# Optimization experiments

Measured on AMD Instinct MI355X. Metric: run time of the kernel, lower is better.

The kernel has to match this reference:

```python
import jax, jax.numpy as jnp
import numpy as np

N, MAX_NB, H, L, V, B, M = 16384, 15, 512, 128, 1024, 256, 65536


def setup_inputs() -> dict:
    key = jax.random.key(0)
    ks = jax.random.split(key, 32)
    s = 0.02  # param init scale
    inp = {
        'x_ids': jax.random.randint(ks[0], (N,), 0, V, dtype=jnp.int32),
        'contexts': jax.random.randint(ks[1], (N,), 0, B, dtype=jnp.int32),
        'nei_idx': jax.random.randint(ks[2], (N, MAX_NB), 0, M, dtype=jnp.int32),
        'nei_mask': jax.random.randint(ks[3], (N, MAX_NB), 0, 2, dtype=jnp.int32),
        'o_idx': jax.random.randint(ks[4], (N, MAX_NB), 0, M, dtype=jnp.int32),
        'o_mask': jax.random.randint(ks[5], (N, MAX_NB), 0, 2, dtype=jnp.int32),
        'H_msg': jax.random.normal(ks[6], (M, H), jnp.float32),
        'x_tree_vecs': jax.random.normal(ks[7], (B, L), jnp.float32),
        'embedding': jax.random.normal(ks[8], (V, H), jnp.float32) * s,
        'Wz_w': jax.random.normal(ks[9], (H, 2 * H), jnp.float32) * s,
        'Wz_b': jnp.zeros((H,), jnp.float32),
        'Wr_w': jax.random.normal(ks[10], (H, H), jnp.float32) * s,
        'Wr_b': jnp.zeros((H,), jnp.float32),
        'Ur_w': jax.random.normal(ks[11], (H, H), jnp.float32) * s,
        'Wh_w': jax.random.normal(ks[12], (H, 2 * H), jnp.float32) * s,
        'Wh_b': jnp.zeros((H,), jnp.float32),
        'W_w': jax.random.normal(ks[13], (H, H + L), jnp.float32) * s,
        'W_b': jnp.zeros((H,), jnp.float32),
        'Wo_w': jax.random.normal(ks[14], (V, H), jnp.float32) * s,
        'Wo_b': jnp.zeros((V,), jnp.float32),
        'Ui_w': jax.random.normal(ks[15], (H, 2 * H), jnp.float32) * s,
        'Ui_b': jnp.zeros((H,), jnp.float32),
        'U_w': jax.random.normal(ks[16], (H, H + L), jnp.float32) * s,
        'U_b': jnp.zeros((H,), jnp.float32),
        'Uo_w': jax.random.normal(ks[17], (1, H), jnp.float32) * s,
        'Uo_b': jnp.zeros((1,), jnp.float32),
    }
    return inp


def _gru(x, h_nei, Wz_w, Wz_b, Wr_w, Wr_b, Ur_w, Wh_w, Wh_b):
    # x: [N,H], h_nei: [N,MAX_NB,H]
    sum_h = h_nei.sum(axis=1)
    z = jax.nn.sigmoid(jnp.concatenate([x, sum_h], axis=1) @ Wz_w.T + Wz_b)
    r1 = (x @ Wr_w.T + Wr_b)[:, None, :]          # [N,1,H]
    r2 = jnp.einsum('nkh,gh->nkg', h_nei, Ur_w)   # U_r(h_nei), no bias
    r = jax.nn.sigmoid(r1 + r2)
    sum_gated = (r * h_nei).sum(axis=1)
    pre_h = jnp.tanh(jnp.concatenate([x, sum_gated], axis=1) @ Wh_w.T + Wh_b)
    return (1.0 - z) * sum_h + z * pre_h


def reference(x_ids, contexts, nei_idx, nei_mask, o_idx, o_mask, H_msg,
              x_tree_vecs, embedding, Wz_w, Wz_b, Wr_w, Wr_b, Ur_w,
              Wh_w, Wh_b, W_w, W_b, Wo_w, Wo_b, Ui_w, Ui_b, U_w, U_b,
              Uo_w, Uo_b):
    x = embedding[x_ids]                                   # [N,H]
    h_nei = H_msg[nei_idx] * nei_mask[..., None].astype(H_msg.dtype)  # [N,NB,H]
    o_nei = H_msg[o_idx] * o_mask[..., None].astype(H_msg.dtype)
    new_h = _gru(x, h_nei, Wz_w, Wz_b, Wr_w, Wr_b, Ur_w, Wh_w, Wh_b)
    cur_o = o_nei.sum(axis=1)                              # [N,H]
    ctx = x_tree_vecs[contexts]                            # [N,L]
    # word prediction: aggregate(new_h, contexts, x_tree_vecs, 'word')
    w_hid = jax.nn.relu(jnp.concatenate([new_h, ctx], axis=1) @ W_w.T + W_b)
    word_scores = w_hid @ Wo_w.T + Wo_b                    # [N,V]
    # stop prediction: U_i(cat(x, cur_o)) -> aggregate(..., 'stop')
    stop_h = jax.nn.relu(jnp.concatenate([x, cur_o], axis=1) @ Ui_w.T + Ui_b)
    s_hid = jax.nn.relu(jnp.concatenate([stop_h, ctx], axis=1) @ U_w.T + U_b)
    stop_scores = s_hid @ Uo_w.T + Uo_b                    # [N,1]
    return jnp.concatenate([word_scores, stop_scores], axis=1)  # [N,V+1]
```

## Files before the change

kernel.cpp:

```cpp
#include <hip/hip_runtime.h>
#include <hip/hip_bf16.h>

typedef unsigned short u16;
typedef unsigned int u32;
typedef __attribute__((ext_vector_type(8))) short s8v;
typedef __attribute__((ext_vector_type(4))) float f4v;

#define HDIM 512
#define NNODE 16384
#define NB 15

__device__ __forceinline__ u16 f2bu(float x) {
  union { float f; u32 i; } v; v.f = x;
  u32 r = v.i + 0x7FFFu + ((v.i >> 16) & 1u);
  return (u16)(r >> 16);
}
__device__ __forceinline__ float bu2f(u16 u) {
  union { u32 i; float f; } v; v.i = ((u32)u) << 16;
  return v.f;
}
__device__ __forceinline__ u32 pk(float a, float b) {
  return (u32)f2bu(a) | ((u32)f2bu(b) << 16);
}
__device__ __forceinline__ float sigm(float x) {
  return __builtin_amdgcn_rcpf(1.f + __expf(-x));
}
__device__ __forceinline__ void gl16(const void* g, void* l) {
  __builtin_amdgcn_global_load_lds(
      (const __attribute__((address_space(1))) u32*)g,
      (__attribute__((address_space(3))) u32*)l, 16, 0, 0);
}
template<int N> __device__ __forceinline__ void wait_vm() {
  if constexpr (N == 0) asm volatile("s_waitcnt vmcnt(0)" ::: "memory");
  else if constexpr (N == 2) asm volatile("s_waitcnt vmcnt(2)" ::: "memory");
  else asm volatile("s_waitcnt vmcnt(4)" ::: "memory");
}

__global__ __launch_bounds__(256) void k_cvt_all(
    const float* Wz_w, const float* Wr_w, const float* Wh_w, const float* Ui_w,
    const float* Ur_w, const float* W_w, const float* U_w, const float* Wo_w,
    const float* emb, const float* xtree,
    const float* Wz_b, const float* Wr_b, const float* Wh_b, const float* Ui_b,
    const float* W_b, const float* U_b,
    u16* wcat, u16* wz_h, u16* wh_h, u16* ui_h, u16* ur, u16* w_n, u16* u_n,
    u16* ccat, u16* wo, u16* emb_bf, u16* xt_bf, float* ebias, float* cbias) {
  int seg = blockIdx.y;
  const float* src = nullptr; u16* dst = nullptr;
  const float* fsrc = nullptr; float* fdst = nullptr;
  int R = 0, Cs = 0, c0 = 0, C = 0, fn = 0;
  switch (seg) {
    case 0:  src = Wz_w; dst = wcat;              R = 512;  Cs = 1024; c0 = 0;   C = 512; break;
    case 1:  src = Wr_w; dst = wcat + 512 * 512;  R = 512;  Cs = 512;  c0 = 0;   C = 512; break;
    case 2:  src = Wh_w; dst = wcat + 1024 * 512; R = 512;  Cs = 1024; c0 = 0;   C = 512; break;
    case 3:  src = Ui_w; dst = wcat + 1536 * 512; R = 512;  Cs = 1024; c0 = 0;   C = 512; break;
    case 4:  src = Wz_w; dst = wz_h;              R = 512;  Cs = 1024; c0 = 512; C = 512; break;
    case 5:  src = Wh_w; dst = wh_h;              R = 512;  Cs = 1024; c0 = 512; C = 512; break;
    case 6:  src = Ui_w; dst = ui_h;              R = 512;  Cs = 1024; c0 = 512; C = 512; break;
    case 7:  src = Ur_w; dst = ur;                R = 512;  Cs = 512;  c0 = 0;   C = 512; break;
    case 8:  src = W_w;  dst = w_n;               R = 512;  Cs = 640;  c0 = 0;   C = 512; break;
    case 9:  src = U_w;  dst = u_n;               R = 512;  Cs = 640;  c0 = 0;   C = 512; break;
    case 10: src = W_w;  dst = ccat;              R = 512;  Cs = 640;  c0 = 512; C = 128; break;
    case 11: src = U_w;  dst = ccat + 512 * 128;  R = 512;  Cs = 640;  c0 = 512; C = 128; break;
    case 12: src = Wo_w; dst = wo;                R = 1024; Cs = 512;  c0 = 0;   C = 512; break;
    case 13: src = emb;  dst = emb_bf;            R = 1024; Cs = 512;  c0 = 0;   C = 512; break;
    case 14: src = xtree; dst = xt_bf;            R = 256;  Cs = 128;  c0 = 0;   C = 128; break;
    case 15: fsrc = Wz_b; fdst = ebias;        fn = 512; break;
    case 16: fsrc = Wr_b; fdst = ebias + 512;  fn = 512; break;
    case 17: fsrc = Wh_b; fdst = ebias + 1024; fn = 512; break;
    case 18: fsrc = Ui_b; fdst = ebias + 1536; fn = 512; break;
    case 19: fsrc = W_b;  fdst = cbias;        fn = 512; break;
    case 20: fsrc = U_b;  fdst = cbias + 512;  fn = 512; break;
  }
  int i = blockIdx.x * 256 + threadIdx.x;
  if (fdst) { if (i < fn) fdst[i] = fsrc[i]; return; }
  int e0 = i * 8;
  if (e0 >= R * C) return;
  int r = e0 / C, c = e0 - r * C;
  const float* s = src + (size_t)r * Cs + c0 + c;
  float4 a = *reinterpret_cast<const float4*>(s);
  float4 b = *reinterpret_cast<const float4*>(s + 4);
  uint4 o = {pk(a.x, a.y), pk(a.z, a.w), pk(b.x, b.y), pk(b.z, b.w)};
  *reinterpret_cast<uint4*>(&dst[e0]) = o;
}

__global__ void k_cvtH(const float* __restrict__ src, u16* __restrict__ HR) {
  size_t i = ((size_t)blockIdx.x * 256 + threadIdx.x) * 8;
  size_t m = i >> 9, c = i & 511;
  float4 a = *reinterpret_cast<const float4*>(src + i);
  float4 b = *reinterpret_cast<const float4*>(src + i + 4);
  uint4 o = {pk(a.x, a.y), pk(a.z, a.w), pk(b.x, b.y), pk(b.z, b.w)};
  *reinterpret_cast<uint4*>(&HR[m * 1024 + c]) = o;
}

struct GP {
  const u16* A; const u16* B; int K; int lda;
  const float* gadd; int ldg; const int* gidx;
  const float* bias; const u16* shb;
  float* outf; u16* outh; int ldo;
};

template<int EP>
__device__ __forceinline__ void epi(int row, int col, float v, const GP& g) {
  if constexpr (EP == 0) {
    g.outf[(size_t)row * g.ldo + col] = v + (g.bias ? g.bias[col] : 0.f);
  } else if constexpr (EP == 3) {
    float pre = v + g.gadd[(size_t)g.gidx[row] * g.ldg + col];
    g.outh[(size_t)row * g.ldo + col] = f2bu(pre > 0.f ? pre : 0.f);
  } else {
    g.outh[(size_t)row * g.ldo + col] = f2bu(v);
  }
}

template<int EP, int KV>
__device__ void gemm_core(const GP& g, u16* AsB, u16* BsB) {
  const int tid = threadIdx.x, lane = tid & 63, w = tid >> 6;
  const int wm = (w >> 2) * 64, wn = (w & 3) * 32;
  const int nx = gridDim.x;
  int orig = blockIdx.y * nx + blockIdx.x;
  int q = (nx * gridDim.y) >> 3;
  int tile = (orig & 7) * q + (orig >> 3);
  const int n0 = (tile % nx) * 128, m0 = (tile / nx) * 128;

  const int sr = tid >> 2, sc = (tid & 3) ^ ((sr >> 1) & 3);
  const u16* gA = g.A + (size_t)(m0 + sr) * g.lda + sc * 8;
  const u16* gB = g.B + (size_t)(n0 + sr) * KV + sc * 8;
  const int ls = tid * 8;

  f4v acc[4][2];
  f4v z4 = {0.f, 0.f, 0.f, 0.f};
#pragma unroll
  for (int a = 0; a < 4; a++) { acc[a][0] = z4; acc[a][1] = z4; }

  constexpr int T = KV / 32;
  auto STAGE = [&](int t) {
    int buf = (t & 3) * 4096;
    gl16(gA + t * 32, AsB + buf + ls);
    gl16(gB + t * 32, BsB + buf + ls);
  };
  STAGE(0); STAGE(1); STAGE(2);

#pragma unroll
  for (int t = 0; t < T; t++) {
    if (t < T - 2) wait_vm<4>();
    else if (t == T - 2) wait_vm<2>();
    else wait_vm<0>();
    __builtin_amdgcn_s_barrier();
    asm volatile("" ::: "memory");
    if (t + 3 < T) STAGE(t + 3);
    const u16* as = AsB + (t & 3) * 4096;
    const u16* bs = BsB + (t & 3) * 4096;
    s8v af[4], bf[2];
    int cc = lane >> 4;
#pragma unroll
    for (int i = 0; i < 4; i++) {
      int R = wm + i * 16 + (lane & 15);
      af[i] = *reinterpret_cast<const s8v*>(
          &as[R * 32 + (cc ^ ((R >> 1) & 3)) * 8]);
    }
#pragma unroll
    for (int i = 0; i < 2; i++) {
      int C = wn + i * 16 + (lane & 15);
      bf[i] = *reinterpret_cast<const s8v*>(
          &bs[C * 32 + (cc ^ ((C >> 1) & 3)) * 8]);
    }
    __builtin_amdgcn_s_setprio(1);
#pragma unroll
    for (int mi = 0; mi < 4; mi++)
#pragma unroll
      for (int ni = 0; ni < 2; ni++)
        acc[mi][ni] = __builtin_amdgcn_mfma_f32_16x16x32_bf16(
            af[mi], bf[ni], acc[mi][ni], 0, 0, 0);
    __builtin_amdgcn_s_setprio(0);
  }
#pragma unroll
  for (int mi = 0; mi < 4; mi++)
#pragma unroll
    for (int ni = 0; ni < 2; ni++)
#pragma unroll
      for (int r = 0; r < 4; r++) {
        int row = m0 + wm + mi * 16 + (lane >> 4) * 4 + r;
        int col = n0 + wn + ni * 16 + (lane & 15);
        epi<EP>(row, col, acc[mi][ni][r], g);
      }
}

template<int EP, int KV>
__global__ __launch_bounds__(512, 4) void k_gemm(GP g) {
  __shared__ u16 As[4 * 4096], Bs[4 * 4096];
  gemm_core<EP, KV>(g, As, Bs);
}

template<int EPa, int EPb, int KV>
__global__ __launch_bounds__(512, 4) void k_pair(GP a, GP b) {
  __shared__ u16 As[4 * 4096], Bs[4 * 4096];
  if (blockIdx.z == 0) gemm_core<EPa, KV>(a, As, Bs);
  else gemm_core<EPb, KV>(b, As, Bs);
}

__global__ __launch_bounds__(512, 4) void k_znp(
    const u16* __restrict__ sumh, const u16* __restrict__ sg,
    const u16* __restrict__ Wz, const u16* __restrict__ Wh,
    const float* __restrict__ E_z, const float* __restrict__ E_h, int ldg,
    const int* __restrict__ gidx, u16* __restrict__ newh, GP gs) {
  __shared__ u16 S[32768];
  if (blockIdx.z == 1) { gemm_core<3, 512>(gs, S, S + 16384); return; }
  const int tid = threadIdx.x, lane = tid & 63, w = tid >> 6;
  const int wm = (w >> 2) * 64, wn = (w & 3) * 32;
  const int nx = gridDim.x;
  int orig = blockIdx.y * nx + blockIdx.x;
  int q = (nx * gridDim.y) >> 3;
  int tile = (orig & 7) * q + (orig >> 3);
  const int n0 = (tile % nx) * 128, m0 = (tile / nx) * 128;

  const int sr = tid >> 2, sc = (tid & 3) ^ ((sr >> 1) & 3);
  const u16* gA1 = sumh + (size_t)(m0 + sr) * HDIM + sc * 8;
  const u16* gA2 = sg + (size_t)(m0 + sr) * HDIM + sc * 8;
  const u16* gB1 = Wz + (size_t)(n0 + sr) * HDIM + sc * 8;
  const u16* gB2 = Wh + (size_t)(n0 + sr) * HDIM + sc * 8;
  const int ls = tid * 8;
  auto STAGE = [&](int t) {
    u16* base = S + (t & 1) * 16384;
    int k0 = t * 32;
    gl16(gA1 + k0, base + ls);
    gl16(gB1 + k0, base + 4096 + ls);
    gl16(gA2 + k0, base + 8192 + ls);
    gl16(gB2 + k0, base + 12288 + ls);
  };

  f4v az[4][2], ah[4][2];
  f4v z4 = {0.f, 0.f, 0.f, 0.f};
#pragma unroll
  for (int a = 0; a < 4; a++) {
    az[a][0] = z4; az[a][1] = z4; ah[a][0] = z4; ah[a][1] = z4;
  }

  STAGE(0);
#pragma unroll
  for (int t = 0; t < 16; t++) {
    __syncthreads();
    if (t + 1 < 16) STAGE(t + 1);
    const u16* base = S + (t & 1) * 16384;
    const u16* As1 = base, *Bs1 = base + 4096;
    const u16* As2 = base + 8192, *Bs2 = base + 12288;
    int cc = lane >> 4;
    {
      s8v af[4], bf[2];
#pragma unroll
      for (int i = 0; i < 4; i++) {
        int R = wm + i * 16 + (lane & 15);
        af[i] = *reinterpret_cast<const s8v*>(
            &As1[R * 32 + (cc ^ ((R >> 1) & 3)) * 8]);
      }
#pragma unroll
      for (int i = 0; i < 2; i++) {
        int C = wn + i * 16 + (lane & 15);
        bf[i] = *reinterpret_cast<const s8v*>(
            &Bs1[C * 32 + (cc ^ ((C >> 1) & 3)) * 8]);
      }
      __builtin_amdgcn_s_setprio(1);
#pragma unroll
      for (int mi = 0; mi < 4; mi++)
#pragma unroll
        for (int ni = 0; ni < 2; ni++)
          az[mi][ni] = __builtin_amdgcn_mfma_f32_16x16x32_bf16(
              af[mi], bf[ni], az[mi][ni], 0, 0, 0);
      __builtin_amdgcn_s_setprio(0);
    }
    {
      s8v af[4], bf[2];
#pragma unroll
      for (int i = 0; i < 4; i++) {
        int R = wm + i * 16 + (lane & 15);
        af[i] = *reinterpret_cast<const s8v*>(
            &As2[R * 32 + (cc ^ ((R >> 1) & 3)) * 8]);
      }
#pragma unroll
      for (int i = 0; i < 2; i++) {
        int C = wn + i * 16 + (lane & 15);
        bf[i] = *reinterpret_cast<const s8v*>(
            &Bs2[C * 32 + (cc ^ ((C >> 1) & 3)) * 8]);
      }
      __builtin_amdgcn_s_setprio(1);
#pragma unroll
      for (int mi = 0; mi < 4; mi++)
#pragma unroll
        for (int ni = 0; ni < 2; ni++)
          ah[mi][ni] = __builtin_amdgcn_mfma_f32_16x16x32_bf16(
              af[mi], bf[ni], ah[mi][ni], 0, 0, 0);
      __builtin_amdgcn_s_setprio(0);
    }
  }
#pragma unroll
  for (int mi = 0; mi < 4; mi++)
#pragma unroll
    for (int r = 0; r < 4; r++) {
      int row = m0 + wm + mi * 16 + (lane >> 4) * 4 + r;
      int xid = gidx[row];
      const float* ez = E_z + (size_t)xid * ldg;
      const float* eh = E_h + (size_t)xid * ldg;
#pragma unroll
      for (int ni = 0; ni < 2; ni++) {
        int col = n0 + wn + ni * 16 + (lane & 15);
        float zv = sigm(az[mi][ni][r] + ez[col]);
        float pre = tanhf(ah[mi][ni][r] + eh[col]);
        float sh = bu2f(sumh[(size_t)row * HDIM + col]);
        newh[(size_t)row * HDIM + col] = f2bu((1.f - zv) * sh + zv * pre);
      }
    }
}

__global__ __launch_bounds__(256) void k_gsr(
    const u16* __restrict__ HR,
    const float* __restrict__ E_r, int ldg, const int* __restrict__ x_ids,
    const int* __restrict__ nei_idx, const int* __restrict__ nei_mask,
    const int* __restrict__ o_idx, const int* __restrict__ o_mask,
    u16* __restrict__ sum_h_bf, u16* __restrict__ sg_bf,
    u16* __restrict__ cur_o_bf) {
  int t = threadIdx.x;
  int nd = t >> 6, lane = t & 63;
  int n = blockIdx.x * 4 + nd;
  __shared__ int sidx[4][NB], smsk[4][NB], soid[4][NB], somk[4][NB];
  __shared__ int sx[4];
  if (t < 60) {
    int nn = t / 15, k = t - nn * 15;
    size_t gofs = (size_t)(blockIdx.x * 4 + nn) * NB + k;
    sidx[nn][k] = nei_idx[gofs];
    smsk[nn][k] = nei_mask[gofs];
  } else if (t >= 64 && t < 124) {
    int tt = t - 64;
    int nn = tt / 15, k = tt - nn * 15;
    size_t gofs = (size_t)(blockIdx.x * 4 + nn) * NB + k;
    soid[nn][k] = o_idx[gofs];
    somk[nn][k] = o_mask[gofs];
  } else if (t >= 128 && t < 132) {
    sx[t - 128] = x_ids[blockIdx.x * 4 + (t - 128)];
  }
  __syncthreads();
  int c = lane * 8;
  const float* er = E_r + (size_t)sx[nd] * ldg + c;
  float4 e0 = *reinterpret_cast<const float4*>(er);
  float4 e1 = *reinterpret_cast<const float4*>(er + 4);
  float ev[8] = {e0.x, e0.y, e0.z, e0.w, e1.x, e1.y, e1.z, e1.w};
  float s[8], gg[8], oo[8];
#pragma unroll
  for (int i = 0; i < 8; i++) { s[i] = 0.f; gg[i] = 0.f; oo[i] = 0.f; }
#pragma unroll
  for (int k = 0; k < NB; k++) {
    if (smsk[nd][k]) {
      const u16* row = HR + (size_t)sidx[nd][k] * 1024 + c;
      uint4 hv = *reinterpret_cast<const uint4*>(row);
      uint4 rv = *reinterpret_cast<const uint4*>(row + 512);
      u32 ha[4] = {hv.x, hv.y, hv.z, hv.w};
      u32 ra[4] = {rv.x, rv.y, rv.z, rv.w};
#pragma unroll
      for (int p = 0; p < 4; p++) {
        float h0 = bu2f((u16)ha[p]), h1 = bu2f((u16)(ha[p] >> 16));
        s[p * 2] += h0; s[p * 2 + 1] += h1;
        gg[p * 2] += sigm(bu2f((u16)ra[p]) + ev[p * 2]) * h0;
        gg[p * 2 + 1] += sigm(bu2f((u16)(ra[p] >> 16)) + ev[p * 2 + 1]) * h1;
      }
    }
    if (somk[nd][k]) {
      uint4 ov = *reinterpret_cast<const uint4*>(
          HR + (size_t)soid[nd][k] * 1024 + c);
      u32 oa[4] = {ov.x, ov.y, ov.z, ov.w};
#pragma unroll
      for (int p = 0; p < 4; p++) {
        oo[p * 2] += bu2f((u16)oa[p]);
        oo[p * 2 + 1] += bu2f((u16)(oa[p] >> 16));
      }
    }
  }
  size_t b = (size_t)n * HDIM + c;
  uint4 ps = {pk(s[0], s[1]), pk(s[2], s[3]), pk(s[4], s[5]), pk(s[6], s[7])};
  uint4 pg = {pk(gg[0], gg[1]), pk(gg[2], gg[3]), pk(gg[4], gg[5]), pk(gg[6], gg[7])};
  uint4 po = {pk(oo[0], oo[1]), pk(oo[2], oo[3]), pk(oo[4], oo[5]), pk(oo[6], oo[7])};
  *reinterpret_cast<uint4*>(&sum_h_bf[b]) = ps;
  *reinterpret_cast<uint4*>(&sg_bf[b]) = pg;
  *reinterpret_cast<uint4*>(&cur_o_bf[b]) = po;
}

__global__ __launch_bounds__(512, 4) void k_wordstop(
    GP wgp, const u16* __restrict__ shid, const float* __restrict__ Uo_w,
    const float* __restrict__ Uo_b, float* __restrict__ out) {
  __shared__ u16 As[4 * 4096], Bs[4 * 4096];
  if (blockIdx.z == 0) { gemm_core<0, 512>(wgp, As, Bs); return; }
  int b = blockIdx.y * gridDim.x + blockIdx.x;
  int wv = threadIdx.x >> 6, lane = threadIdx.x & 63;
#pragma unroll
  for (int i = 0; i < 2; i++) {
    int n = b * 16 + wv * 2 + i;
    const u16* row = shid + (size_t)n * HDIM + lane * 8;
    const float* uw = Uo_w + lane * 8;
    uint4 v = *reinterpret_cast<const uint4*>(row);
    float4 u0 = *reinterpret_cast<const float4*>(uw);
    float4 u1 = *reinterpret_cast<const float4*>(uw + 4);
    float s = bu2f((u16)v.x) * u0.x + bu2f((u16)(v.x >> 16)) * u0.y +
              bu2f((u16)v.y) * u0.z + bu2f((u16)(v.y >> 16)) * u0.w +
              bu2f((u16)v.z) * u1.x + bu2f((u16)(v.z >> 16)) * u1.y +
              bu2f((u16)v.w) * u1.z + bu2f((u16)(v.w >> 16)) * u1.w;
#pragma unroll
    for (int off = 32; off; off >>= 1) s += __shfl_xor(s, off, 64);
    if (lane == 0) out[(size_t)n * 1025 + 1024] = s + Uo_b[0];
  }
}

extern "C" void kernel_launch(void* const* d_in, const int* in_sizes, int n_in,
                              void* d_out, int out_size, void* d_ws, size_t ws_size,
                              hipStream_t stream) {
  const int* x_ids = (const int*)d_in[0];
  const int* contexts = (const int*)d_in[1];
  const int* nei_idx = (const int*)d_in[2];
  const int* nei_mask = (const int*)d_in[3];
  const int* o_idx = (const int*)d_in[4];
  const int* o_mask = (const int*)d_in[5];
  const float* H_msg = (const float*)d_in[6];
  const float* xtree = (const float*)d_in[7];
  const float* emb = (const float*)d_in[8];
  const float* Wz_w = (const float*)d_in[9];  const float* Wz_b = (const float*)d_in[10];
  const float* Wr_w = (const float*)d_in[11]; const float* Wr_b = (const float*)d_in[12];
  const float* Ur_w = (const float*)d_in[13];
  const float* Wh_w = (const float*)d_in[14]; const float* Wh_b = (const float*)d_in[15];
  const float* W_w  = (const float*)d_in[16]; const float* W_b  = (const float*)d_in[17];
  const float* Wo_w = (const float*)d_in[18]; const float* Wo_b = (const float*)d_in[19];
  const float* Ui_w = (const float*)d_in[20]; const float* Ui_b = (const float*)d_in[21];
  const float* U_w  = (const float*)d_in[22]; const float* U_b  = (const float*)d_in[23];
  const float* Uo_w = (const float*)d_in[24]; const float* Uo_b = (const float*)d_in[25];
  float* out = (float*)d_out;
  const int M = 65536;

  char* base = (char*)d_ws;
  size_t ofs = 0;
  auto alloc = [&](size_t bytes) -> char* {
    char* p = base + ofs;
    ofs = (ofs + bytes + 255) & ~(size_t)255;
    return p;
  };
  u16* wcat  = (u16*)alloc((size_t)2048 * 512 * 2);
  u16* wz_h  = (u16*)alloc(512 * 512 * 2);
  u16* wh_h  = (u16*)alloc(512 * 512 * 2);
  u16* ui_h  = (u16*)alloc(512 * 512 * 2);
  u16* ur    = (u16*)alloc(512 * 512 * 2);
  u16* w_n   = (u16*)alloc(512 * 512 * 2);
  u16* u_n   = (u16*)alloc(512 * 512 * 2);
  u16* ccat  = (u16*)alloc(1024 * 128 * 2);
  u16* wo    = (u16*)alloc(1024 * 512 * 2);
  u16* emb_bf = (u16*)alloc(1024 * 512 * 2);
  u16* xt_bf  = (u16*)alloc(256 * 128 * 2);
  float* ebias = (float*)alloc(2048 * 4);
  float* cbias = (float*)alloc(1024 * 4);
  float* E_cat = (float*)alloc((size_t)1024 * 2048 * 4);
  float* C_cat = (float*)alloc((size_t)256 * 1024 * 4);
  u16* HR = (u16*)alloc((size_t)M * 1024 * 2);
  u16* sum_h_bf = (u16*)alloc((size_t)NNODE * HDIM * 2);
  u16* cur_o_bf = (u16*)alloc((size_t)NNODE * HDIM * 2);
  u16* sg_bf    = (u16*)alloc((size_t)NNODE * HDIM * 2);
  u16* newh_bf  = (u16*)alloc((size_t)NNODE * HDIM * 2);
  u16* whid_bf  = (u16*)alloc((size_t)NNODE * HDIM * 2);
  u16* stoph_bf = (u16*)alloc((size_t)NNODE * HDIM * 2);
  u16* shid_bf  = (u16*)alloc((size_t)NNODE * HDIM * 2);

  k_cvt_all<<<dim3(256, 21), dim3(256), 0, stream>>>(
      Wz_w, Wr_w, Wh_w, Ui_w, Ur_w, W_w, U_w, Wo_w, emb, xtree,
      Wz_b, Wr_b, Wh_b, Ui_b, W_b, U_b,
      wcat, wz_h, wh_h, ui_h, ur, w_n, u_n, ccat, wo, emb_bf, xt_bf,
      ebias, cbias);
  k_cvtH<<<dim3(16384), dim3(256), 0, stream>>>(H_msg, HR);

  GP ge{emb_bf, wcat, 512, 512, nullptr, 0, nullptr, ebias, nullptr,
        E_cat, nullptr, 2048};
  k_gemm<0, 512><<<dim3(16, 8), dim3(512), 0, stream>>>(ge);
  GP gc{xt_bf, ccat, 128, 128, nullptr, 0, nullptr, cbias, nullptr,
        C_cat, nullptr, 1024};
  k_gemm<0, 128><<<dim3(8, 2), dim3(512), 0, stream>>>(gc);

  GP gr{HR, ur, 512, 1024, nullptr, 0, nullptr, nullptr, nullptr,
        nullptr, HR + 512, 1024};
  k_gemm<4, 512><<<dim3(4, 512), dim3(512), 0, stream>>>(gr);

  k_gsr<<<dim3(NNODE / 4), dim3(256), 0, stream>>>(
      HR, E_cat + 512, 2048, x_ids, nei_idx, nei_mask, o_idx, o_mask,
      sum_h_bf, sg_bf, cur_o_bf);

  GP gs{cur_o_bf, ui_h, 512, 512, E_cat + 1536, 2048, x_ids, nullptr, nullptr,
        nullptr, stoph_bf, 512};
  k_znp<<<dim3(4, 128, 2), dim3(512), 0, stream>>>(
      sum_h_bf, sg_bf, wz_h, wh_h, E_cat, E_cat + 1024, 2048, x_ids,
      newh_bf, gs);

  GP gw{newh_bf, w_n, 512, 512, C_cat, 1024, contexts, nullptr, nullptr,
        nullptr, whid_bf, 512};
  GP gu{stoph_bf, u_n, 512, 512, C_cat + 512, 1024, contexts, nullptr, nullptr,
        nullptr, shid_bf, 512};
  k_pair<3, 3, 512><<<dim3(4, 128, 2), dim3(512), 0, stream>>>(gw, gu);

  GP gword{whid_bf, wo, 512, 512, nullptr, 0, nullptr, Wo_b, nullptr,
           out, nullptr, 1025};
  k_wordstop<<<dim3(8, 128, 2), dim3(512), 0, stream>>>(
      gword, shid_bf, Uo_w, Uo_b, out);
}
```

Measured before the change: 315.8 us.

## Pipeline z/h GEMM loads as 4-stage ring with vmcnt waits

Reworks the dual-GEMM main loop in k_znp from a double-buffered 16-step loop into a 32-step loop that alternates the z and h operand pairs. Each step's tile goes into a 4-slot shared-memory ring, with three stages in flight. Explicit vmcnt waits plus raw barriers replace __syncthreads, so global loads overlap deeper with MFMA work. The trade-off is finer-grained barriers (twice as many) and reliance on wait_vm counts being correct for the async load pattern.

```diff
diff --git a/kernel.cpp b/kernel.cpp
--- a/kernel.cpp
+++ b/kernel.cpp
@@ -213,18 +213,18 @@
   const int n0 = (tile % nx) * 128, m0 = (tile / nx) * 128;
 
   const int sr = tid >> 2, sc = (tid & 3) ^ ((sr >> 1) & 3);
-  const u16* gA1 = sumh + (size_t)(m0 + sr) * HDIM + sc * 8;
-  const u16* gA2 = sg + (size_t)(m0 + sr) * HDIM + sc * 8;
-  const u16* gB1 = Wz + (size_t)(n0 + sr) * HDIM + sc * 8;
-  const u16* gB2 = Wh + (size_t)(n0 + sr) * HDIM + sc * 8;
+  const u16* gA[2] = {sumh + (size_t)(m0 + sr) * HDIM + sc * 8,
+                      sg + (size_t)(m0 + sr) * HDIM + sc * 8};
+  const u16* gB[2] = {Wz + (size_t)(n0 + sr) * HDIM + sc * 8,
+                      Wh + (size_t)(n0 + sr) * HDIM + sc * 8};
   const int ls = tid * 8;
-  auto STAGE = [&](int t) {
-    u16* base = S + (t & 1) * 16384;
-    int k0 = t * 32;
-    gl16(gA1 + k0, base + ls);
-    gl16(gB1 + k0, base + 4096 + ls);
-    gl16(gA2 + k0, base + 8192 + ls);
-    gl16(gB2 + k0, base + 12288 + ls);
+  u16* AsB = S;
+  u16* BsB = S + 16384;
+  auto STAGE = [&](int s) {
+    int p = s & 1, k0 = (s >> 1) * 32;
+    int buf = (s & 3) * 4096;
+    gl16(gA[p] + k0, AsB + buf + ls);
+    gl16(gB[p] + k0, BsB + buf + ls);
   };
 
   f4v az[4][2], ah[4][2];
@@ -234,61 +234,40 @@
     az[a][0] = z4; az[a][1] = z4; ah[a][0] = z4; ah[a][1] = z4;
   }
 
-  STAGE(0);
-#pragma unroll
-  for (int t = 0; t < 16; t++) {
-    __syncthreads();
-    if (t + 1 < 16) STAGE(t + 1);
-    const u16* base = S + (t & 1) * 16384;
-    const u16* As1 = base, *Bs1 = base + 4096;
-    const u16* As2 = base + 8192, *Bs2 = base + 12288;
+  STAGE(0); STAGE(1); STAGE(2);
+#pragma unroll
+  for (int s = 0; s < 32; s++) {
+    if (s < 30) wait_vm<4>();
+    else if (s == 30) wait_vm<2>();
+    else wait_vm<0>();
+    __builtin_amdgcn_s_barrier();
+    asm volatile("" ::: "memory");
+    if (s + 3 < 32) STAGE(s + 3);
+    const u16* as = AsB + (s & 3) * 4096;
+    const u16* bs = BsB + (s & 3) * 4096;
+    s8v af[4], bf[2];
     int cc = lane >> 4;
-    {
-      s8v af[4], bf[2];
-#pragma unroll
-      for (int i = 0; i < 4; i++) {
-        int R = wm + i * 16 + (lane & 15);
-        af[i] = *reinterpret_cast<const s8v*>(
-            &As1[R * 32 + (cc ^ ((R >> 1) & 3)) * 8]);
-      }
-#pragma unroll
-      for (int i = 0; i < 2; i++) {
-        int C = wn + i * 16 + (lane & 15);
-        bf[i] = *reinterpret_cast<const s8v*>(
-            &Bs1[C * 32 + (cc ^ ((C >> 1) & 3)) * 8]);
-      }
-      __builtin_amdgcn_s_setprio(1);
-#pragma unroll
-      for (int mi = 0; mi < 4; mi++)
-#pragma unroll
-        for (int ni = 0; ni < 2; ni++)
-          az[mi][ni] = __builtin_amdgcn_mfma_f32_16x16x32_bf16(
-              af[mi], bf[ni], az[mi][ni], 0, 0, 0);
-      __builtin_amdgcn_s_setprio(0);
-    }
-    {
-      s8v af[4], bf[2];
-#pragma unroll
-      for (int i = 0; i < 4; i++) {
-        int R = wm + i * 16 + (lane & 15);
-        af[i] = *reinterpret_cast<const s8v*>(
-            &As2[R * 32 + (cc ^ ((R >> 1) & 3)) * 8]);
-      }
-#pragma unroll
-      for (int i = 0; i < 2; i++) {
-        int C = wn + i * 16 + (lane & 15);
-        bf[i] = *reinterpret_cast<const s8v*>(
-            &Bs2[C * 32 + (cc ^ ((C >> 1) & 3)) * 8]);
-      }
-      __builtin_amdgcn_s_setprio(1);
-#pragma unroll
-      for (int mi = 0; mi < 4; mi++)
-#pragma unroll
-        for (int ni = 0; ni < 2; ni++)
-          ah[mi][ni] = __builtin_amdgcn_mfma_f32_16x16x32_bf16(
-              af[mi], bf[ni], ah[mi][ni], 0, 0, 0);
-      __builtin_amdgcn_s_setprio(0);
-    }
+#pragma unroll
+    for (int i = 0; i < 4; i++) {
+      int R = wm + i * 16 + (lane & 15);
+      af[i] = *reinterpret_cast<const s8v*>(
+          &as[R * 32 + (cc ^ ((R >> 1) & 3)) * 8]);
+    }
+#pragma unroll
+    for (int i = 0; i < 2; i++) {
+      int C = wn + i * 16 + (lane & 15);
+      bf[i] = *reinterpret_cast<const s8v*>(
+          &bs[C * 32 + (cc ^ ((C >> 1) & 3)) * 8]);
+    }
+    f4v (&acc)[4][2] = (s & 1) ? ah : az;
+    __builtin_amdgcn_s_setprio(1);
+#pragma unroll
+    for (int mi = 0; mi < 4; mi++)
+#pragma unroll
+      for (int ni = 0; ni < 2; ni++)
+        acc[mi][ni] = __builtin_amdgcn_mfma_f32_16x16x32_bf16(
+            af[mi], bf[ni], acc[mi][ni], 0, 0, 0);
+    __builtin_amdgcn_s_setprio(0);
   }
 #pragma unroll
   for (int mi = 0; mi < 4; mi++)
```

Result: no change. 314.6 us (-0.4%).
